# Kernel tuning notes

Measured on AMD Instinct MI355X. Metric: run time of the kernel, lower is better.

Reference implementation:

```python
import jax, jax.numpy as jnp
import numpy as np

B, S, D_IN = 4, 256, 1024
ATTN, HD = 1024, 64
H = ATTN // HD  # 16
C = 4096          # n_classes
R, CR, SC = 256, 1024, 2048  # n_roots, n_classroots, n_subclasses
FF = int(ATTN * 3.0)  # 3072
EPS = 1e-5


def setup_inputs() -> dict:
    key = jax.random.key(0)
    ks = jax.random.split(key, 16)
    x = jax.random.normal(ks[0], (B, S, D_IN), dtype=jnp.float32)
    cls = jax.random.normal(ks[1], (H, C, HD), dtype=jnp.float32)
    roots = jax.random.normal(ks[2], (H, R, HD), dtype=jnp.float32)
    # IndexedAdd indices: row 0 selects from src, row 1 scatters into dst
    clsroots_idx = jnp.stack([
        jax.random.randint(ks[3], (CR,), 0, R, dtype=jnp.int32),
        jax.random.randint(ks[4], (CR,), 0, C, dtype=jnp.int32)])
    clscls_idx = jnp.stack([
        jax.random.randint(ks[5], (SC,), 0, C, dtype=jnp.int32),
        jax.random.randint(ks[6], (SC,), 0, C, dtype=jnp.int32)])
    clsroots_w = jax.random.uniform(ks[7], (H, CR, 1), dtype=jnp.float32, minval=0.5, maxval=1.5)
    clscls_w = jax.random.uniform(ks[8], (H, SC, 1), dtype=jnp.float32, minval=0.5, maxval=1.5)
    sc = 1.0 / np.sqrt(D_IN)
    kv_w = jax.random.uniform(ks[9], (2 * ATTN, D_IN), dtype=jnp.float32, minval=-sc, maxval=sc)
    ln_gamma = jnp.ones((ATTN,), dtype=jnp.float32)
    ln_beta = jnp.zeros((ATTN,), dtype=jnp.float32)
    sa = 1.0 / np.sqrt(ATTN)
    ff_in_w = jax.random.uniform(ks[10], (2 * FF, ATTN), dtype=jnp.float32, minval=-sa, maxval=sa)
    sf = 1.0 / np.sqrt(FF)
    ff_out_w = jax.random.uniform(ks[11], (ATTN, FF), dtype=jnp.float32, minval=-sf, maxval=sf)
    out_w = jax.random.uniform(ks[12], (C, ATTN, 2), dtype=jnp.float32, minval=-sa, maxval=sa)
    return {"x": x, "cls": cls, "roots": roots, "clsroots_w": clsroots_w,
            "clscls_w": clscls_w, "kv_w": kv_w, "ln_gamma": ln_gamma, "ln_beta": ln_beta,
            "ff_in_w": ff_in_w, "ff_out_w": ff_out_w, "out_w": out_w,
            "clsroots_idx": clsroots_idx, "clscls_idx": clscls_idx}


def _rmsnorm(t):
    return t * jax.lax.rsqrt(jnp.mean(t * t, axis=-1, keepdims=True) + EPS)


def _silu(t):
    return t * jax.nn.sigmoid(t)


def reference(x, cls, roots, clsroots_w, clscls_w, kv_w, ln_gamma, ln_beta,
              ff_in_w, ff_out_w, out_w, clsroots_idx, clscls_idx):
    # --- hierarchical query build (IndexedAdd chain) ---
    qr = _rmsnorm(roots)                                        # [H,R,E]
    q = cls.at[:, clsroots_idx[1], :].add(qr[:, clsroots_idx[0], :] * clsroots_w)
    q_det = jax.lax.stop_gradient(q)                            # clscls uses q.detach()
    q = q.at[:, clscls_idx[1], :].add(q_det[:, clscls_idx[0], :] * clscls_w)
    q = _rmsnorm(q)                                             # [H,C,E]
    # --- KV projection + QK-RMSNorm cross-attention ---
    kv = (x @ kv_w.T).reshape(B, S, 2, H, HD)                   # '(n h e)' split
    k = jnp.transpose(kv[:, :, 0], (0, 2, 1, 3))                # [B,H,S,E]
    v = jnp.transpose(kv[:, :, 1], (0, 2, 1, 3))                # [B,H,S,E]
    k = _rmsnorm(k)
    scores = jnp.einsum('hce,bhse->bhcs', q, k) / np.sqrt(HD)   # [B,H,C,S]
    attn = jax.nn.softmax(scores, axis=-1)
    o = jnp.einsum('bhcs,bhse->bhce', attn, v)                  # [B,H,C,E]
    o = jnp.transpose(o, (0, 2, 1, 3)).reshape(B, C, ATTN)      # [B,C,ATTN]
    # --- SwiGLU FFN with pre-LayerNorm + residual ---
    mu = jnp.mean(o, axis=-1, keepdims=True)
    var = jnp.mean((o - mu) ** 2, axis=-1, keepdims=True)
    f = (o - mu) * jax.lax.rsqrt(var + EPS) * ln_gamma + ln_beta
    f = f @ ff_in_w.T                                           # [B,C,2*FF]
    f1, f2 = f[..., :FF], f[..., FF:]
    h = (_silu(f1) * f2) @ ff_out_w.T
    z = o + h                                                   # [B,C,ATTN]
    # --- per-class BatchLinear + SwiGLU output ---
    y = jnp.einsum('bca,cao->bco', z, out_w)                    # [B,C,2]
    out = _silu(y[..., 0:1]) * y[..., 1:2]                      # [B,C,1]
    return out
```

## Files before the change

### kernel.cpp

```cpp
#include <hip/hip_runtime.h>
#include <math.h>

#define EPS 1e-5f

typedef __bf16 bf16x8 __attribute__((ext_vector_type(8)));
typedef __bf16 bf16x4 __attribute__((ext_vector_type(4)));
typedef float f32x4 __attribute__((ext_vector_type(4)));

#define GPTR(p) ((const __attribute__((address_space(1))) void*)(p))
#define LPTR(p) ((__attribute__((address_space(3))) void*)(p))

__device__ __forceinline__ float wave_sum(float v) {
#pragma unroll
    for (int o = 32; o; o >>= 1) v += __shfl_xor(v, o);
    return v;
}

__global__ __launch_bounds__(256) void scatter1(const float* __restrict__ roots,
                                                const float* __restrict__ w,
                                                const int* __restrict__ idx,
                                                float* __restrict__ q) {
    int unit = (blockIdx.x << 2) + (threadIdx.x >> 6);
    int lane = threadIdx.x & 63;
    int h = unit >> 10;
    int i = unit & 1023;
    int r = idx[i];
    int c = idx[1024 + i];
    float val = roots[(h * 256 + r) * 64 + lane];
    float ss = wave_sum(val * val);
    float rs = rsqrtf(ss * (1.f / 64.f) + EPS);
    atomicAdd(&q[(h * 4096 + c) * 64 + lane], val * rs * w[(h << 10) + i]);
}

__global__ __launch_bounds__(256) void scatter2(const float* __restrict__ qdet,
                                                const float* __restrict__ w,
                                                const int* __restrict__ idx,
                                                float* __restrict__ q) {
    int unit = (blockIdx.x << 2) + (threadIdx.x >> 6);
    int lane = threadIdx.x & 63;
    int h = unit >> 11;
    int i = unit & 2047;
    int c1 = idx[i];
    int c2 = idx[2048 + i];
    float val = qdet[(h * 4096 + c1) * 64 + lane] * w[(h << 11) + i];
    atomicAdd(&q[(h * 4096 + c2) * 64 + lane], val);
}

__global__ __launch_bounds__(256) void rms_q_bf(const float* __restrict__ q,
                                                __bf16* __restrict__ qb) {
    int unit = (blockIdx.x << 2) + (threadIdx.x >> 6);
    int lane = threadIdx.x & 63;
    float v = q[(size_t)unit * 64 + lane];
    float ss = wave_sum(v * v);
    float r = v * rsqrtf(ss * (1.f / 64.f) + EPS);
    qb[(size_t)unit * 64 + lane] = (__bf16)r;
}

__global__ __launch_bounds__(256) void split8(const float* __restrict__ in,
                                              __bf16* __restrict__ hi,
                                              __bf16* __restrict__ lo, int n8) {
    int i = blockIdx.x * 256 + threadIdx.x;
    if (i >= n8) return;
    const float4* p = (const float4*)in + (size_t)i * 2;
    float4 u0 = p[0], u1 = p[1];
    float f[8] = {u0.x, u0.y, u0.z, u0.w, u1.x, u1.y, u1.z, u1.w};
    bf16x8 vh, vl;
#pragma unroll
    for (int j = 0; j < 8; ++j) {
        vh[j] = (__bf16)f[j];
        vl[j] = (__bf16)(f[j] - (float)vh[j]);
    }
    *((bf16x8*)hi + i) = vh;
    *((bf16x8*)lo + i) = vl;
}

__global__ __launch_bounds__(256) void gemm_kv_mfma(const __bf16* __restrict__ Ah,
                                                    const __bf16* __restrict__ Al,
                                                    const __bf16* __restrict__ Bh,
                                                    const __bf16* __restrict__ Bl,
                                                    float* __restrict__ Cout) {
    __shared__ __bf16 sAh[64 * 64], sAl[64 * 64];
    __shared__ __bf16 sBh[128 * 64], sBl[128 * 64];
    int tid = threadIdx.x;
    int bn = blockIdx.x, bm = blockIdx.y;
    int lane = tid & 63;
    int w = tid >> 6;
    int wr = (w >> 1) * 32, wc = (w & 1) * 64;
    int frow = lane & 15, fk = (lane >> 4) * 8;
    f32x4 acc[2][4] = {};
    const __bf16* Ahb = Ah + (size_t)(bm * 64) * 1024;
    const __bf16* Alb = Al + (size_t)(bm * 64) * 1024;
    const __bf16* Bhb = Bh + (size_t)(bn * 128) * 1024;
    const __bf16* Blb = Bl + (size_t)(bn * 128) * 1024;
    for (int k0 = 0; k0 < 1024; k0 += 64) {
#pragma unroll
        for (int t = 0; t < 2; ++t) {
            int e = (t * 256 + tid) * 8;
            int r = e >> 6, c = e & 63;
            __builtin_amdgcn_global_load_lds(GPTR(Ahb + (size_t)r * 1024 + k0 + c), LPTR(sAh + e), 16, 0, 0);
            __builtin_amdgcn_global_load_lds(GPTR(Alb + (size_t)r * 1024 + k0 + c), LPTR(sAl + e), 16, 0, 0);
        }
#pragma unroll
        for (int t = 0; t < 4; ++t) {
            int e = (t * 256 + tid) * 8;
            int r = e >> 6, c = e & 63;
            __builtin_amdgcn_global_load_lds(GPTR(Bhb + (size_t)r * 1024 + k0 + c), LPTR(sBh + e), 16, 0, 0);
            __builtin_amdgcn_global_load_lds(GPTR(Blb + (size_t)r * 1024 + k0 + c), LPTR(sBl + e), 16, 0, 0);
        }
        __syncthreads();
#pragma unroll
        for (int ks = 0; ks < 2; ++ks) {
            bf16x8 ah[2], al[2], bh2[4], bl2[4];
#pragma unroll
            for (int m = 0; m < 2; ++m) {
                ah[m] = *(const bf16x8*)(sAh + (wr + m * 16 + frow) * 64 + ks * 32 + fk);
                al[m] = *(const bf16x8*)(sAl + (wr + m * 16 + frow) * 64 + ks * 32 + fk);
            }
#pragma unroll
            for (int n = 0; n < 4; ++n) {
                bh2[n] = *(const bf16x8*)(sBh + (wc + n * 16 + frow) * 64 + ks * 32 + fk);
                bl2[n] = *(const bf16x8*)(sBl + (wc + n * 16 + frow) * 64 + ks * 32 + fk);
            }
#pragma unroll
            for (int m = 0; m < 2; ++m)
#pragma unroll
                for (int n = 0; n < 4; ++n) {
                    acc[m][n] = __builtin_amdgcn_mfma_f32_16x16x32_bf16(ah[m], bh2[n], acc[m][n], 0, 0, 0);
                    acc[m][n] = __builtin_amdgcn_mfma_f32_16x16x32_bf16(ah[m], bl2[n], acc[m][n], 0, 0, 0);
                    acc[m][n] = __builtin_amdgcn_mfma_f32_16x16x32_bf16(al[m], bh2[n], acc[m][n], 0, 0, 0);
                }
        }
        __syncthreads();
    }
    int crow = (lane >> 4) * 4, ccol = lane & 15;
#pragma unroll
    for (int m = 0; m < 2; ++m)
#pragma unroll
        for (int n = 0; n < 4; ++n)
#pragma unroll
            for (int j = 0; j < 4; ++j) {
                int row = bm * 64 + wr + m * 16 + crow + j;
                int col = bn * 128 + wc + n * 16 + ccol;
                Cout[(size_t)row * 2048 + col] = acc[m][n][j];
            }
}

__global__ __launch_bounds__(256) void kvsplit_bf(const float* __restrict__ kv,
                                                  __bf16* __restrict__ kb) {
    int unit = (blockIdx.x << 2) + (threadIdx.x >> 6);
    int lane = threadIdx.x & 63;
    int b = unit >> 12;
    int h = (unit >> 8) & 15;
    int s = unit & 255;
    float kvl = kv[(size_t)(b * 256 + s) * 2048 + (h << 6) + lane];
    float ss = wave_sum(kvl * kvl);
    float kn = kvl * rsqrtf(ss * (1.f / 64.f) + EPS);
    kb[(size_t)unit * 64 + lane] = (__bf16)kn;
}

__global__ __launch_bounds__(256) void vtrans_bf(const float* __restrict__ kv,
                                                 __bf16* __restrict__ vt) {
    __shared__ float T[64][65];
    int bh = blockIdx.x >> 2;
    int sc = blockIdx.x & 3;
    int b = bh >> 4, h = bh & 15;
    int tid = threadIdx.x;
    int s0 = sc * 64;
    int sl = tid >> 2, d0 = (tid & 3) * 16;
    const float* src = kv + (size_t)(b * 256 + s0 + sl) * 2048 + 1024 + (h << 6) + d0;
#pragma unroll
    for (int t = 0; t < 4; ++t) {
        float4 v4 = *(const float4*)(src + t * 4);
        T[sl][d0 + t * 4 + 0] = v4.x;
        T[sl][d0 + t * 4 + 1] = v4.y;
        T[sl][d0 + t * 4 + 2] = v4.z;
        T[sl][d0 + t * 4 + 3] = v4.w;
    }
    __syncthreads();
    int dr = tid >> 2, c0 = (tid & 3) * 16;
    bf16x8 h0, h1;
#pragma unroll
    for (int jj = 0; jj < 8; ++jj) h0[jj] = (__bf16)T[c0 + jj][dr];
#pragma unroll
    for (int jj = 0; jj < 8; ++jj) h1[jj] = (__bf16)T[c0 + 8 + jj][dr];
    size_t base = (size_t)bh * 16384 + (size_t)dr * 256 + s0 + c0;
    *(bf16x8*)(vt + base) = h0;
    *(bf16x8*)(vt + base + 8) = h1;
}

__global__ __launch_bounds__(256) void attn_mfma(const __bf16* __restrict__ qb,
                                                 const __bf16* __restrict__ kb,
                                                 const __bf16* __restrict__ vtb,
                                                 __bf16* __restrict__ ob) {
    __shared__ __bf16 P[64 * 264];
    __shared__ float wred[8][64];
    __shared__ float denomL[64];
    __shared__ __bf16 Ot[64 * 72];

    int wg = blockIdx.x;
    int swz = (wg & 7) * 512 + (wg >> 3);
    int bh = swz >> 6;
    int qt = swz & 63;
    int b = bh >> 4, h = bh & 15;
    int tid = threadIdx.x;
    int lane = tid & 63;
    int w = tid >> 6;
    int frow = lane & 15;
    int fk = (lane >> 4) * 8;
    int crow = (lane >> 4) * 4;
    int ccol = lane & 15;
    int q0 = qt * 64;
    int wsr = w * 64;

    const __bf16* kh = kb + (size_t)bh * 16384;
    const __bf16* qh = qb + (size_t)h * 262144 + (size_t)q0 * 64;

    f32x4 acc[4][4] = {};
#pragma unroll
    for (int ks = 0; ks < 2; ++ks) {
        bf16x8 kf[4];
#pragma unroll
        for (int m = 0; m < 4; ++m)
            kf[m] = *(const bf16x8*)(kh + (wsr + m * 16 + frow) * 64 + ks * 32 + fk);
#pragma unroll
        for (int n = 0; n < 4; ++n) {
            bf16x8 qf = *(const bf16x8*)(qh + (n * 16 + frow) * 64 + ks * 32 + fk);
#pragma unroll
            for (int m = 0; m < 4; ++m)
                acc[m][n] = __builtin_amdgcn_mfma_f32_16x16x32_bf16(kf[m], qf, acc[m][n], 0, 0, 0);
        }
    }
#pragma unroll
    for (int m = 0; m < 4; ++m)
#pragma unroll
        for (int n = 0; n < 4; ++n)
#pragma unroll
            for (int j = 0; j < 4; ++j) acc[m][n][j] *= 0.125f;

    float lm[4];
#pragma unroll
    for (int n = 0; n < 4; ++n) {
        float v = -1e30f;
#pragma unroll
        for (int m = 0; m < 4; ++m)
#pragma unroll
            for (int j = 0; j < 4; ++j) v = fmaxf(v, acc[m][n][j]);
        v = fmaxf(v, __shfl_xor(v, 16));
        v = fmaxf(v, __shfl_xor(v, 32));
        lm[n] = v;
    }
    if (lane < 16) {
#pragma unroll
        for (int n = 0; n < 4; ++n) wred[w][n * 16 + lane] = lm[n];
    }
    __syncthreads();
    float gm[4];
#pragma unroll
    for (int n = 0; n < 4; ++n) {
        int qq = n * 16 + ccol;
        gm[n] = fmaxf(fmaxf(wred[0][qq], wred[1][qq]), fmaxf(wred[2][qq], wred[3][qq]));
    }
    float lsum[4] = {0.f, 0.f, 0.f, 0.f};
#pragma unroll
    for (int m = 0; m < 4; ++m)
#pragma unroll
        for (int n = 0; n < 4; ++n)
#pragma unroll
            for (int j = 0; j < 4; ++j) {
                float p = __expf(acc[m][n][j] - gm[n]);
                acc[m][n][j] = p;
                lsum[n] += p;
            }
#pragma unroll
    for (int n = 0; n < 4; ++n) {
        float v = lsum[n];
        v += __shfl_xor(v, 16);
        v += __shfl_xor(v, 32);
        lsum[n] = v;
    }
    if (lane < 16) {
#pragma unroll
        for (int n = 0; n < 4; ++n) wred[4 + w][n * 16 + lane] = lsum[n];
    }
#pragma unroll
    for (int m = 0; m < 4; ++m)
#pragma unroll
        for (int n = 0; n < 4; ++n) {
            bf16x4 pv;
#pragma unroll
            for (int j = 0; j < 4; ++j) pv[j] = (__bf16)acc[m][n][j];
            *(bf16x4*)(P + (n * 16 + ccol) * 264 + wsr + m * 16 + crow) = pv;
        }
    __syncthreads();
    if (tid < 64)
        denomL[tid] = wred[4][tid] + wred[5][tid] + wred[6][tid] + wred[7][tid];

    const __bf16* vh = vtb + (size_t)bh * 16384;
    f32x4 accO[4] = {};
#pragma unroll
    for (int ks = 0; ks < 8; ++ks) {
        bf16x8 pf = *(const bf16x8*)(P + (w * 16 + frow) * 264 + ks * 32 + fk);
#pragma unroll
        for (int m = 0; m < 4; ++m) {
            bf16x8 vf = *(const bf16x8*)(vh + (m * 16 + frow) * 256 + ks * 32 + fk);
            accO[m] = __builtin_amdgcn_mfma_f32_16x16x32_bf16(vf, pf, accO[m], 0, 0, 0);
        }
    }
    __syncthreads();
    float rd = 1.0f / denomL[w * 16 + ccol];
#pragma unroll
    for (int m = 0; m < 4; ++m) {
        bf16x4 ov;
#pragma unroll
        for (int j = 0; j < 4; ++j) ov[j] = (__bf16)(accO[m][j] * rd);
        *(bf16x4*)(Ot + (w * 16 + ccol) * 72 + m * 16 + crow) = ov;
    }
    __syncthreads();
    {
        int qq = tid >> 2, dc = tid & 3;
        bf16x8 o0 = *(const bf16x8*)(Ot + qq * 72 + dc * 16);
        bf16x8 o1 = *(const bf16x8*)(Ot + qq * 72 + dc * 16 + 8);
        size_t base = (size_t)((b << 12) + q0 + qq) * 1024 + (h << 6) + dc * 16;
        *(bf16x8*)(ob + base) = o0;
        *(bf16x8*)(ob + base + 8) = o1;
    }
}

__global__ __launch_bounds__(256) void cvt_bf16(const float* __restrict__ in,
                                                __bf16* __restrict__ out, int n8) {
    int i = blockIdx.x * 256 + threadIdx.x;
    if (i >= n8) return;
    const float4* p = (const float4*)in + (size_t)i * 2;
    float4 u0 = p[0], u1 = p[1];
    bf16x8 v;
    v[0] = (__bf16)u0.x; v[1] = (__bf16)u0.y; v[2] = (__bf16)u0.z; v[3] = (__bf16)u0.w;
    v[4] = (__bf16)u1.x; v[5] = (__bf16)u1.y; v[6] = (__bf16)u1.z; v[7] = (__bf16)u1.w;
    *((bf16x8*)out + i) = v;
}

__global__ __launch_bounds__(256) void ln_stats(const __bf16* __restrict__ ob,
                                                float* __restrict__ mu,
                                                float* __restrict__ rstd) {
    __shared__ float r0[4], r1[4];
    int row = blockIdx.x;
    int tid = threadIdx.x;
    const bf16x4* op = (const bf16x4*)(ob + (size_t)row * 1024);
    bf16x4 v = op[tid];
    float s = 0, sq = 0;
#pragma unroll
    for (int j = 0; j < 4; ++j) { float f = (float)v[j]; s += f; sq += f * f; }
    s = wave_sum(s);
    sq = wave_sum(sq);
    if ((tid & 63) == 0) { r0[tid >> 6] = s; r1[tid >> 6] = sq; }
    __syncthreads();
    if (tid == 0) {
        float S = r0[0] + r0[1] + r0[2] + r0[3];
        float Q = r1[0] + r1[1] + r1[2] + r1[3];
        float m = S * (1.f / 1024.f);
        float var = Q * (1.f / 1024.f) - m * m;
        mu[row] = m;
        rstd[row] = rsqrtf(var + EPS);
    }
}

__global__ __launch_bounds__(256) void ln_apply(const __bf16* __restrict__ ob,
                                                const float* __restrict__ mu,
                                                const float* __restrict__ rstd,
                                                const float* __restrict__ gamma,
                                                const float* __restrict__ beta,
                                                __bf16* __restrict__ f, int R0) {
    int i = blockIdx.x * 256 + threadIdx.x;
    int row = i >> 7;
    int c8 = (i & 127) * 8;
    int gr = R0 + row;
    float m = mu[gr], rs = rstd[gr];
    bf16x8 ov = *((const bf16x8*)(ob + (size_t)gr * 1024 + c8));
    bf16x8 r;
#pragma unroll
    for (int j = 0; j < 8; ++j) {
        float v = (float)ov[j];
        r[j] = (__bf16)((v - m) * rs * gamma[c8 + j] + beta[c8 + j]);
    }
    *((bf16x8*)(f + (size_t)row * 1024 + c8)) = r;
}

__global__ __launch_bounds__(256) void gemm1_mfma(const __bf16* __restrict__ A,
                                                  const __bf16* __restrict__ W,
                                                  __bf16* __restrict__ U) {
    __shared__ __align__(16) unsigned char smemraw[32768];
    __bf16* sA = (__bf16*)smemraw;
    __bf16* sB = (__bf16*)(smemraw + 16384);
    float* sEx = (float*)smemraw;
    const int K = 1024;
    int tid = threadIdx.x;
    int bn = blockIdx.x, bm = blockIdx.y;
    int lane = tid & 63;
    int w = tid >> 6;
    int wr = (w >> 1) * 64, wc = (w & 1) * 64;
    f32x4 acc[4][4] = {};
    const __bf16* Ab = A + (size_t)(bm * 128) * K;
    const __bf16* B1b = W + (size_t)(bn * 64) * K;
    const __bf16* B2b = W + (size_t)(3072 + bn * 64) * K;
    int frow = lane & 15, fk = (lane >> 4) * 8;
    for (int k0 = 0; k0 < K; k0 += 64) {
#pragma unroll
        for (int t = 0; t < 4; ++t) {
            int e = (t * 256 + tid) * 8;
            int r = e >> 6, c = e & 63;
            __builtin_amdgcn_global_load_lds(GPTR(Ab + (size_t)r * K + k0 + c), LPTR(sA + e), 16, 0, 0);
        }
#pragma unroll
        for (int t = 0; t < 2; ++t) {
            int e = (t * 256 + tid) * 8;
            int r = e >> 6, c = e & 63;
            __builtin_amdgcn_global_load_lds(GPTR(B1b + (size_t)r * K + k0 + c), LPTR(sB + e), 16, 0, 0);
        }
#pragma unroll
        for (int t = 2; t < 4; ++t) {
            int e = (t * 256 + tid) * 8;
            int r = (e >> 6) - 64, c = e & 63;
            __builtin_amdgcn_global_load_lds(GPTR(B2b + (size_t)r * K + k0 + c), LPTR(sB + e), 16, 0, 0);
        }
        __syncthreads();
#pragma unroll
        for (int ks = 0; ks < 2; ++ks) {
            bf16x8 a[4], b[4];
#pragma unroll
            for (int m = 0; m < 4; ++m)
                a[m] = *(const bf16x8*)(sA + (wr + m * 16 + frow) * 64 + ks * 32 + fk);
#pragma unroll
            for (int n = 0; n < 4; ++n)
                b[n] = *(const bf16x8*)(sB + (wc + n * 16 + frow) * 64 + ks * 32 + fk);
#pragma unroll
            for (int m = 0; m < 4; ++m)
#pragma unroll
                for (int n = 0; n < 4; ++n)
                    acc[m][n] = __builtin_amdgcn_mfma_f32_16x16x32_bf16(a[m], b[n], acc[m][n], 0, 0, 0);
        }
        __syncthreads();
    }
    int crow = (lane >> 4) * 4, ccol = lane & 15;
    if ((w & 1) == 0) {
#pragma unroll
        for (int m = 0; m < 4; ++m)
#pragma unroll
            for (int n = 0; n < 4; ++n)
#pragma unroll
                for (int j = 0; j < 4; ++j)
                    sEx[(wr + m * 16 + crow + j) * 64 + n * 16 + ccol] = acc[m][n][j];
    }
    __syncthreads();
    if (w & 1) {
#pragma unroll
        for (int m = 0; m < 4; ++m)
#pragma unroll
            for (int n = 0; n < 4; ++n)
#pragma unroll
                for (int j = 0; j < 4; ++j) {
                    int row = wr + m * 16 + crow + j;
                    int col = n * 16 + ccol;
                    float f1 = sEx[row * 64 + col];
                    float f2 = acc[m][n][j];
                    float sg = f1 / (1.f + expf(-f1));
                    U[(size_t)(bm * 128 + row) * 3072 + bn * 64 + col] = (__bf16)(sg * f2);
                }
    }
}

__global__ __launch_bounds__(256) void gemm2_mfma(const __bf16* __restrict__ U,
                                                  const __bf16* __restrict__ W2,
                                                  __bf16* __restrict__ Oz) {
    __shared__ __bf16 sA[64 * 64];
    __shared__ __bf16 sB[128 * 64];
    const int K = 3072;
    int tid = threadIdx.x;
    int bn = blockIdx.x, bm = blockIdx.y;
    int lane = tid & 63;
    int w = tid >> 6;
    int wr = (w >> 1) * 32, wc = (w & 1) * 64;
    f32x4 acc[2][4] = {};
    const __bf16* Ab = U + (size_t)(bm * 64) * K;
    const __bf16* Bb = W2 + (size_t)(bn * 128) * K;
    int frow = lane & 15, fk = (lane >> 4) * 8;
    for (int k0 = 0; k0 < K; k0 += 64) {
#pragma unroll
        for (int t = 0; t < 2; ++t) {
            int e = (t * 256 + tid) * 8;
            int r = e >> 6, c = e & 63;
            __builtin_amdgcn_global_load_lds(GPTR(Ab + (size_t)r * K + k0 + c), LPTR(sA + e), 16, 0, 0);
        }
#pragma unroll
        for (int t = 0; t < 4; ++t) {
            int e = (t * 256 + tid) * 8;
            int r = e >> 6, c = e & 63;
            __builtin_amdgcn_global_load_lds(GPTR(Bb + (size_t)r * K + k0 + c), LPTR(sB + e), 16, 0, 0);
        }
        __syncthreads();
#pragma unroll
        for (int ks = 0; ks < 2; ++ks) {
            bf16x8 a[2], b[4];
#pragma unroll
            for (int m = 0; m < 2; ++m)
                a[m] = *(const bf16x8*)(sA + (wr + m * 16 + frow) * 64 + ks * 32 + fk);
#pragma unroll
            for (int n = 0; n < 4; ++n)
                b[n] = *(const bf16x8*)(sB + (wc + n * 16 + frow) * 64 + ks * 32 + fk);
#pragma unroll
            for (int m = 0; m < 2; ++m)
#pragma unroll
                for (int n = 0; n < 4; ++n)
                    acc[m][n] = __builtin_amdgcn_mfma_f32_16x16x32_bf16(a[m], b[n], acc[m][n], 0, 0, 0);
        }
        __syncthreads();
    }
    int crow = (lane >> 4) * 4, ccol = lane & 15;
#pragma unroll
    for (int m = 0; m < 2; ++m)
#pragma unroll
        for (int n = 0; n < 4; ++n)
#pragma unroll
            for (int j = 0; j < 4; ++j) {
                int row = bm * 64 + wr + m * 16 + crow + j;
                int col = bn * 128 + wc + n * 16 + ccol;
                size_t off = (size_t)row * 1024 + col;
                float z = (float)Oz[off] + acc[m][n][j];
                Oz[off] = (__bf16)z;
            }
}

__global__ __launch_bounds__(256) void out_proj4(const __bf16* __restrict__ z,
                                                 const float* __restrict__ ow,
                                                 float* __restrict__ out) {
    __shared__ float red[4][8];
    int c = blockIdx.x;
    int tid = threadIdx.x;
    int a0 = tid * 4;
    const float4* w4 = (const float4*)(ow + (size_t)c * 2048);
    float4 wA = w4[tid * 2];
    float4 wB = w4[tid * 2 + 1];
    float y[8];
#pragma unroll
    for (int jj = 0; jj < 8; ++jj) y[jj] = 0.f;
#pragma unroll
    for (int bb = 0; bb < 4; ++bb) {
        bf16x4 zv = *(const bf16x4*)(z + (size_t)((bb << 12) + c) * 1024 + a0);
        float z0 = (float)zv[0], z1 = (float)zv[1], z2 = (float)zv[2], z3 = (float)zv[3];
        y[2 * bb] += z0 * wA.x + z1 * wA.z + z2 * wB.x + z3 * wB.z;
        y[2 * bb + 1] += z0 * wA.y + z1 * wA.w + z2 * wB.y + z3 * wB.w;
    }
#pragma unroll
    for (int jj = 0; jj < 8; ++jj) y[jj] = wave_sum(y[jj]);
    if ((tid & 63) == 0) {
#pragma unroll
        for (int jj = 0; jj < 8; ++jj) red[tid >> 6][jj] = y[jj];
    }
    __syncthreads();
    if (tid < 4) {
        float a0s = red[0][2 * tid] + red[1][2 * tid] + red[2][2 * tid] + red[3][2 * tid];
        float a1s = red[0][2 * tid + 1] + red[1][2 * tid + 1] + red[2][2 * tid + 1] + red[3][2 * tid + 1];
        out[(size_t)tid * 4096 + c] = a0s / (1.f + expf(-a0s)) * a1s;
    }
}

extern "C" void kernel_launch(void* const* d_in, const int* in_sizes, int n_in,
                              void* d_out, int out_size, void* d_ws, size_t ws_size,
                              hipStream_t stream) {
    const float* x = (const float*)d_in[0];
    const float* cls = (const float*)d_in[1];
    const float* roots = (const float*)d_in[2];
    const float* crw = (const float*)d_in[3];
    const float* ccw = (const float*)d_in[4];
    const float* kv_w = (const float*)d_in[5];
    const float* gamma = (const float*)d_in[6];
    const float* beta = (const float*)d_in[7];
    const float* ffin = (const float*)d_in[8];
    const float* ffout = (const float*)d_in[9];
    const float* ow = (const float*)d_in[10];
    const int* cridx = (const int*)d_in[11];
    const int* ccidx = (const int*)d_in[12];
    float* out = (float*)d_out;

    float* ws = (float*)d_ws;
    float* q = ws;
    float* kvb = ws + 4194304;
    __bf16* kbf = (__bf16*)(ws + 6291456);
    __bf16* vtb = (__bf16*)(ws + 6815744);
    __bf16* o_bf = (__bf16*)(ws + 8388608);
    __bf16* xhi = (__bf16*)(ws + 8388608);
    __bf16* xlo = (__bf16*)(ws + 8912896);
    __bf16* kvwhi = (__bf16*)(ws + 9437184);
    __bf16* kvwlo = (__bf16*)(ws + 10485760);
    float* qdet = ws + 16777216;
    __bf16* qbf = (__bf16*)(ws + 20971520);
    __bf16* w1bf = (__bf16*)ws;
    __bf16* w2bf = (__bf16*)(ws + 3145728);
    float* mu = ws + 4718592;
    float* rstd = mu + 16384;
    __bf16* fbf = (__bf16*)(ws + 16777216);
    __bf16* u_s = (__bf16*)(ws + 18874368);

    hipMemcpyAsync(q, cls, 4194304 * sizeof(float), hipMemcpyDeviceToDevice, stream);
    scatter1<<<4096, 256, 0, stream>>>(roots, crw, cridx, q);
    hipMemcpyAsync(qdet, q, 4194304 * sizeof(float), hipMemcpyDeviceToDevice, stream);
    scatter2<<<8192, 256, 0, stream>>>(qdet, ccw, ccidx, q);
    rms_q_bf<<<16384, 256, 0, stream>>>(q, qbf);
    split8<<<512, 256, 0, stream>>>(x, xhi, xlo, 131072);
    split8<<<1024, 256, 0, stream>>>(kv_w, kvwhi, kvwlo, 262144);
    gemm_kv_mfma<<<dim3(16, 16), 256, 0, stream>>>(xhi, xlo, kvwhi, kvwlo, kvb);
    kvsplit_bf<<<4096, 256, 0, stream>>>(kvb, kbf);
    vtrans_bf<<<256, 256, 0, stream>>>(kvb, vtb);
    attn_mfma<<<4096, 256, 0, stream>>>(qbf, kbf, vtb, o_bf);

    cvt_bf16<<<3072, 256, 0, stream>>>(ffin, w1bf, 786432);
    cvt_bf16<<<1536, 256, 0, stream>>>(ffout, w2bf, 393216);
    ln_stats<<<16384, 256, 0, stream>>>(o_bf, mu, rstd);
    for (int sl = 0; sl < 4; ++sl) {
        int R0 = sl * 4096;
        ln_apply<<<2048, 256, 0, stream>>>(o_bf, mu, rstd, gamma, beta, fbf, R0);
        gemm1_mfma<<<dim3(48, 32), 256, 0, stream>>>(fbf, w1bf, u_s);
        gemm2_mfma<<<dim3(8, 64), 256, 0, stream>>>(u_s, w2bf, o_bf + (size_t)R0 * 1024);
    }
    out_proj4<<<4096, 256, 0, stream>>>(o_bf, ow, out);
}
```

Measured before the change: 900.0 us.

## Drop softmax max-subtraction, alias P/Ot shared buffers, prefetch V fragments

Removes the per-row max reduction and its block barrier from the attention softmax and exponentiates the scaled scores directly. This relies on RMS-normed keys keeping the logits small enough not to overflow. Shared memory for P and Ot is aliased into one buffer with a padded stride of 268, which cuts LDS use and may raise occupancy. The first two k-steps of V fragments are loaded before the barrier to hide global latency. The risk is numeric: without max subtraction, large query norms could overflow exp, and P values stored as bf16 lose relative precision.

```diff
diff --git a/kernel.cpp b/kernel.cpp
--- a/kernel.cpp
+++ b/kernel.cpp
@@ -192,10 +192,12 @@
                                                  const __bf16* __restrict__ kb,
                                                  const __bf16* __restrict__ vtb,
                                                  __bf16* __restrict__ ob) {
-    __shared__ __bf16 P[64 * 264];
-    __shared__ float wred[8][64];
+    const int PST = 268;
+    __shared__ __align__(16) unsigned char smem[64 * 268 * 2];
+    __shared__ float wsum[4][64];
     __shared__ float denomL[64];
-    __shared__ __bf16 Ot[64 * 72];
+    __bf16* P = (__bf16*)smem;
+    __bf16* Ot = (__bf16*)smem;
 
     int wg = blockIdx.x;
     int swz = (wg & 7) * 512 + (wg >> 3);
@@ -214,6 +216,7 @@
 
     const __bf16* kh = kb + (size_t)bh * 16384;
     const __bf16* qh = qb + (size_t)h * 262144 + (size_t)q0 * 64;
+    const __bf16* vh = vtb + (size_t)bh * 16384;
 
     f32x4 acc[4][4] = {};
 #pragma unroll
@@ -230,44 +233,15 @@
                 acc[m][n] = __builtin_amdgcn_mfma_f32_16x16x32_bf16(kf[m], qf, acc[m][n], 0, 0, 0);
         }
     }
+
+    float lsum[4] = {0.f, 0.f, 0.f, 0.f};
 #pragma unroll
     for (int m = 0; m < 4; ++m)
 #pragma unroll
         for (int n = 0; n < 4; ++n)
 #pragma unroll
-            for (int j = 0; j < 4; ++j) acc[m][n][j] *= 0.125f;
-
-    float lm[4];
-#pragma unroll
-    for (int n = 0; n < 4; ++n) {
-        float v = -1e30f;
-#pragma unroll
-        for (int m = 0; m < 4; ++m)
-#pragma unroll
-            for (int j = 0; j < 4; ++j) v = fmaxf(v, acc[m][n][j]);
-        v = fmaxf(v, __shfl_xor(v, 16));
-        v = fmaxf(v, __shfl_xor(v, 32));
-        lm[n] = v;
-    }
-    if (lane < 16) {
-#pragma unroll
-        for (int n = 0; n < 4; ++n) wred[w][n * 16 + lane] = lm[n];
-    }
-    __syncthreads();
-    float gm[4];
-#pragma unroll
-    for (int n = 0; n < 4; ++n) {
-        int qq = n * 16 + ccol;
-        gm[n] = fmaxf(fmaxf(wred[0][qq], wred[1][qq]), fmaxf(wred[2][qq], wred[3][qq]));
-    }
-    float lsum[4] = {0.f, 0.f, 0.f, 0.f};
-#pragma unroll
-    for (int m = 0; m < 4; ++m)
-#pragma unroll
-        for (int n = 0; n < 4; ++n)
-#pragma unroll
             for (int j = 0; j < 4; ++j) {
-                float p = __expf(acc[m][n][j] - gm[n]);
+                float p = __expf(acc[m][n][j] * 0.125f);
                 acc[m][n][j] = p;
                 lsum[n] += p;
             }
@@ -280,7 +254,7 @@
     }
     if (lane < 16) {
 #pragma unroll
-        for (int n = 0; n < 4; ++n) wred[4 + w][n * 16 + lane] = lsum[n];
+        for (int n = 0; n < 4; ++n) wsum[w][n * 16 + lane] = lsum[n];
     }
 #pragma unroll
     for (int m = 0; m < 4; ++m)
@@ -289,17 +263,29 @@
             bf16x4 pv;
 #pragma unroll
             for (int j = 0; j < 4; ++j) pv[j] = (__bf16)acc[m][n][j];
-            *(bf16x4*)(P + (n * 16 + ccol) * 264 + wsr + m * 16 + crow) = pv;
-        }
+            *(bf16x4*)(P + (n * 16 + ccol) * PST + wsr + m * 16 + crow) = pv;
+        }
+    bf16x8 vpre[2][4];
+#pragma unroll
+    for (int ks = 0; ks < 2; ++ks)
+#pragma unroll
+        for (int m = 0; m < 4; ++m)
+            vpre[ks][m] = *(const bf16x8*)(vh + (m * 16 + frow) * 256 + ks * 32 + fk);
     __syncthreads();
     if (tid < 64)
-        denomL[tid] = wred[4][tid] + wred[5][tid] + wred[6][tid] + wred[7][tid];
-
-    const __bf16* vh = vtb + (size_t)bh * 16384;
+        denomL[tid] = wsum[0][tid] + wsum[1][tid] + wsum[2][tid] + wsum[3][tid];
+
     f32x4 accO[4] = {};
 #pragma unroll
-    for (int ks = 0; ks < 8; ++ks) {
-        bf16x8 pf = *(const bf16x8*)(P + (w * 16 + frow) * 264 + ks * 32 + fk);
+    for (int ks = 0; ks < 2; ++ks) {
+        bf16x8 pf = *(const bf16x8*)(P + (w * 16 + frow) * PST + ks * 32 + fk);
+#pragma unroll
+        for (int m = 0; m < 4; ++m)
+            accO[m] = __builtin_amdgcn_mfma_f32_16x16x32_bf16(vpre[ks][m], pf, accO[m], 0, 0, 0);
+    }
+#pragma unroll
+    for (int ks = 2; ks < 8; ++ks) {
+        bf16x8 pf = *(const bf16x8*)(P + (w * 16 + frow) * PST + ks * 32 + fk);
 #pragma unroll
         for (int m = 0; m < 4; ++m) {
             bf16x8 vf = *(const bf16x8*)(vh + (m * 16 + frow) * 256 + ks * 32 + fk);
```

Result: no change. 894.5 us (-0.6%).
